# Performance work log

Hardware: AMD Instinct MI355X
Metric: run time of the kernel (lower is better)

## Reference

```python
import jax, jax.numpy as jnp
import numpy as np

# --- quantization helpers (I-BERT-style symmetric quantization) ---

def _quant_int(x, scale, bit):
    # round(x/scale) clamped to signed `bit`-bit range (SymmetricQuantFunction)
    n = 2 ** (bit - 1) - 1
    return jnp.clip(jnp.round(x / scale), -n - 1, n)


def quant_linear(x, s_x, W, b, weight_bit=8):
    """QuantLinear: per-output-channel symmetric 8-bit weight quant, int GEMM, dequant.
    Returns (output, bias_scaling_factor[out_features])."""
    n = 2 ** (weight_bit - 1) - 1
    w_scale = jnp.maximum(jnp.max(jnp.abs(W), axis=1), 1e-8) / n          # (out,)
    w_int = _quant_int(W, w_scale[:, None], weight_bit)                   # int-valued (out,in)
    b_scale = w_scale * s_x                                               # (out,) broadcasts with scalar s_x
    b_int = jnp.round(b / b_scale)                                        # 32-bit bias, no clamp needed
    x_int = x / s_x                                                       # int-valued activations
    out_int = jnp.einsum('bsi,oi->bso', x_int, w_int) + b_int
    return out_int * b_scale, b_scale


def quant_act(x, bit):
    """QuantAct: per-tensor symmetric requantization to `bit` bits (dynamic min/max)."""
    n = 2 ** (bit - 1) - 1
    scale = jnp.maximum(jnp.max(jnp.abs(x)), 1e-8) / n                    # scalar
    x_int = _quant_int(x, scale, bit)
    return x_int * scale, scale


def int_gelu(x, s):
    """IntGELU (I-BERT): integer 2nd-order polynomial approximation of erf."""
    k = 1.4142
    c0, c1 = -0.2888, -1.769
    c2 = 1.0 / c0
    SHIFT = 14  # 'const' in the original code

    x_int = x / s
    se = s / k  # scaling factor fed to int_erf
    # --- int_erf ---
    b_int = jnp.floor(c1 / se)
    c_int = jnp.floor(c2 / se ** 2)
    sign = jnp.sign(x_int)
    abs_int = jnp.minimum(jnp.abs(x_int), -b_int)
    y_int = sign * ((abs_int + b_int) ** 2 + c_int)
    se2 = se ** 2 * c0
    y_int = jnp.floor(y_int / 2 ** SHIFT)
    se2 = se2 * 2 ** SHIFT
    # --- gelu = x * (erf/2 + 1/2) in integer form ---
    shift_int = jnp.floor(1.0 / se2)
    out_int = x_int * (y_int + shift_int)
    s_out = s * se2 / 2
    return out_int * s_out, s_out


def setup_inputs() -> dict:
    key = jax.random.key(0)
    k_x, k_w1, k_b1, k_w2, k_b2 = jax.random.split(key, 5)
    B, S, D, H = 8, 1024, 768, 3072
    x = jax.random.normal(k_x, (B, S, D), dtype=jnp.float32)
    act_scaling_factor = jnp.full((1,), 0.02, dtype=jnp.float32)
    # pre-quantize x onto its input grid (x arrives already quantized in the real pipeline)
    x = jnp.round(x / act_scaling_factor) * act_scaling_factor
    W1 = jax.random.normal(k_w1, (H, D), dtype=jnp.float32) * 0.02
    b1 = jax.random.normal(k_b1, (H,), dtype=jnp.float32) * 0.02
    W2 = jax.random.normal(k_w2, (D, H), dtype=jnp.float32) * 0.02
    b2 = jax.random.normal(k_b2, (D,), dtype=jnp.float32) * 0.02
    return {"x": x, "act_scaling_factor": act_scaling_factor,
            "W1": W1, "b1": b1, "W2": W2, "b2": b2}


def reference(x, act_scaling_factor, W1, b1, W2, b2):
    s = act_scaling_factor
    h, s = quant_linear(x, s, W1, b1)       # fc1: int8 GEMM + dequant
    h, s = quant_act(h, 8)                  # qact_gelu
    h, s = int_gelu(h, s)                   # IntGELU
    h, s = quant_act(h, 8)                  # qact1 (drop=0.0 -> identity)
    h, s = quant_linear(h, s, W2, b2)       # fc2
    h, s = quant_act(h, 16)                 # qact2 (16-bit)
    return h, s
```

## Files before the change

kernel.cpp:

```cpp
#include <hip/hip_runtime.h>

typedef _Float16 half8  __attribute__((ext_vector_type(8)));
typedef _Float16 half4v __attribute__((ext_vector_type(4)));
typedef unsigned short ushort8 __attribute__((ext_vector_type(8)));
typedef float f32x4 __attribute__((ext_vector_type(4)));

#define M_DIM 8192
#define D_DIM 768
#define H_DIM 3072

#define WS_WSCALE2   16
#define WS_BINT1     (WS_WSCALE2 + 768*4)
#define WS_BSCALE1   (WS_BINT1 + 3072*4)
#define WS_BINT2     (WS_BSCALE1 + 3072*4)
#define WS_BSCALE2   (WS_BINT2 + 768*4)
#define WS_LUT       (WS_BSCALE2 + 768*4)
#define WS_XQ        34560UL
#define WS_WQ1       (WS_XQ  + (size_t)M_DIM*D_DIM*2)
#define WS_WQ2       (WS_WQ1 + (size_t)H_DIM*D_DIM*2)
#define WS_H1        (WS_WQ2 + (size_t)D_DIM*H_DIM*2)
#define WS_XQ2       WS_H1
#define WS_Q1        (WS_H1 + (size_t)M_DIM*H_DIM*4)
#define WS_H2        WS_Q1

__device__ __forceinline__ void gl_lds16(const _Float16* g, _Float16* l) {
  __builtin_amdgcn_global_load_lds(
      (const __attribute__((address_space(1))) void*)g,
      (__attribute__((address_space(3))) void*)l, 16, 0, 0);
}

struct GeluP { float scale1, bintg, cintg, shiftint, s_out; };

__device__ __forceinline__ GeluP gelu_params(float max1) {
  GeluP p;
  p.scale1 = fmaxf(max1, 1e-8f) / 127.0f;
  float se = p.scale1 / 1.4142f;
  p.bintg = floorf(-1.769f / se);
  p.cintg = floorf(((float)(1.0 / -0.2888)) / (se * se));
  float se2 = ((se * se) * -0.2888f) * 16384.0f;
  p.shiftint = floorf(1.0f / se2);
  p.s_out = (p.scale1 * se2) * 0.5f;
  return p;
}

__device__ __forceinline__ float gelu_val(const GeluP& p, float qf) {
  float sg = (qf > 0.f) ? 1.f : ((qf < 0.f) ? -1.f : 0.f);
  float aq = fminf(fabsf(qf), -p.bintg);
  float t = aq + p.bintg;
  float y = sg * (t * t + p.cintg);
  float yf = floorf(y * (1.0f / 16384.0f));
  return (qf * (yf + p.shiftint)) * p.s_out;
}

__global__ __launch_bounds__(256)
void k1_prep(const float* __restrict__ W1, const float* __restrict__ b1,
             const float* __restrict__ W2, const float* __restrict__ sxp,
             _Float16* __restrict__ wq1, _Float16* __restrict__ wq2,
             float* __restrict__ wscale2, float* __restrict__ bint1,
             float* __restrict__ bscale1, unsigned* __restrict__ wsu)
{
  if (blockIdx.x == 0 && threadIdx.x == 0) { wsu[0] = 0u; wsu[1] = 0u; wsu[2] = 0u; }
  int w = blockIdx.x * 4 + (threadIdx.x >> 6);
  int lane = threadIdx.x & 63;
  if (w < H_DIM) {
    const float* row = W1 + (size_t)w * D_DIM;
    f32x4 v[3]; float m = 0.f;
#pragma unroll
    for (int t = 0; t < 3; t++) {
      v[t] = *(const f32x4*)(row + t * 256 + lane * 4);
#pragma unroll
      for (int j = 0; j < 4; j++) m = fmaxf(m, fabsf(v[t][j]));
    }
#pragma unroll
    for (int off = 32; off >= 1; off >>= 1) m = fmaxf(m, __shfl_xor(m, off));
    float wsc = fmaxf(m, 1e-8f) / 127.0f;
    _Float16* orow = wq1 + (size_t)w * D_DIM;
#pragma unroll
    for (int t = 0; t < 3; t++) {
      half4v h;
#pragma unroll
      for (int j = 0; j < 4; j++) {
        float q = fminf(fmaxf(rintf(v[t][j] / wsc), -128.f), 127.f);
        h[j] = (_Float16)q;
      }
      *(half4v*)(orow + t * 256 + lane * 4) = h;
    }
    if (lane == 0) {
      float bs = wsc * sxp[0];
      bint1[w] = rintf(b1[w] / bs);
      bscale1[w] = bs;
    }
  } else {
    int o = w - H_DIM;
    const float* row = W2 + (size_t)o * H_DIM;
    f32x4 v[12]; float m = 0.f;
#pragma unroll
    for (int t = 0; t < 12; t++) {
      v[t] = *(const f32x4*)(row + t * 256 + lane * 4);
#pragma unroll
      for (int j = 0; j < 4; j++) m = fmaxf(m, fabsf(v[t][j]));
    }
#pragma unroll
    for (int off = 32; off >= 1; off >>= 1) m = fmaxf(m, __shfl_xor(m, off));
    float wsc = fmaxf(m, 1e-8f) / 127.0f;
    _Float16* orow = wq2 + (size_t)o * H_DIM;
#pragma unroll
    for (int t = 0; t < 12; t++) {
      half4v h;
#pragma unroll
      for (int j = 0; j < 4; j++) {
        float q = fminf(fmaxf(rintf(v[t][j] / wsc), -128.f), 127.f);
        h[j] = (_Float16)q;
      }
      *(half4v*)(orow + t * 256 + lane * 4) = h;
    }
    if (lane == 0) wscale2[o] = wsc;
  }
}

__global__ __launch_bounds__(256)
void k2_quant_x(const float* __restrict__ x, const float* __restrict__ sxp,
                _Float16* __restrict__ xq, int n4)
{
  float sx = sxp[0];
  int stride = gridDim.x * blockDim.x;
  for (int i = blockIdx.x * blockDim.x + threadIdx.x; i < n4; i += stride) {
    f32x4 v = ((const f32x4*)x)[i];
    half4v h;
#pragma unroll
    for (int j = 0; j < 4; j++) h[j] = (_Float16)(v[j] / sx);
    ((half4v*)xq)[i] = h;
  }
}

__global__ __launch_bounds__(256)
void gemm_q(const _Float16* __restrict__ A, const _Float16* __restrict__ B,
            const float* __restrict__ bint, const float* __restrict__ bscale,
            float* __restrict__ C, unsigned* __restrict__ maxw, int N, int K)
{
  __shared__ _Float16 sA[128 * 32];
  __shared__ _Float16 sB[128 * 32];
  __shared__ float wred[4];
  const int tid = threadIdx.x;
  const int wid = tid >> 6;
  const int lane = tid & 63;
  const int m0 = blockIdx.x * 128;
  const int n0 = blockIdx.y * 128;
  const int wr = (wid >> 1) * 64;
  const int wc = (wid & 1) * 64;
  const int lrow = lane & 15;
  const int lk = (lane >> 4) * 8;
  const int srow = lane >> 2;
  const int schunk = (lane & 3) * 8;

  const _Float16* Ab = A + (size_t)m0 * K;
  const _Float16* Bb = B + (size_t)n0 * K;

  f32x4 acc[4][4];
#pragma unroll
  for (int i = 0; i < 4; i++)
#pragma unroll
    for (int j = 0; j < 4; j++) acc[i][j] = (f32x4){0.f, 0.f, 0.f, 0.f};

  for (int k0 = 0; k0 < K; k0 += 32) {
#pragma unroll
    for (int r = 0; r < 2; r++) {
      const int rq = r * 4 + wid;
      const int row = rq * 16 + srow;
      gl_lds16(Ab + (size_t)row * K + (k0 + schunk), sA + rq * 512);
      gl_lds16(Bb + (size_t)row * K + (k0 + schunk), sB + rq * 512);
    }
    __syncthreads();
    half8 a[4], b[4];
#pragma unroll
    for (int f = 0; f < 4; f++) {
      a[f] = *(const half8*)&sA[(wr + f * 16 + lrow) * 32 + lk];
      b[f] = *(const half8*)&sB[(wc + f * 16 + lrow) * 32 + lk];
    }
#pragma unroll
    for (int i = 0; i < 4; i++)
#pragma unroll
      for (int j = 0; j < 4; j++)
        acc[i][j] = __builtin_amdgcn_mfma_f32_16x16x32_f16(a[i], b[j], acc[i][j], 0, 0, 0);
    __syncthreads();
  }

  float tmax = 0.f;
  const int orow0 = m0 + wr + (lane >> 4) * 4;
  const int ocol0 = n0 + wc + lrow;
#pragma unroll
  for (int j = 0; j < 4; j++) {
    const int col = ocol0 + j * 16;
    const float bi = bint[col];
    const float bs = bscale[col];
#pragma unroll
    for (int i = 0; i < 4; i++) {
#pragma unroll
      for (int e = 0; e < 4; e++) {
        const int rowm = orow0 + i * 16 + e;
        float v = (acc[i][j][e] + bi) * bs;
        C[(size_t)rowm * N + col] = v;
        tmax = fmaxf(tmax, fabsf(v));
      }
    }
  }
#pragma unroll
  for (int off = 32; off >= 1; off >>= 1) tmax = fmaxf(tmax, __shfl_xor(tmax, off));
  if (lane == 0) wred[wid] = tmax;
  __syncthreads();
  if (tid == 0) {
    float bm = fmaxf(fmaxf(wred[0], wred[1]), fmaxf(wred[2], wred[3]));
    atomicMax(maxw, __float_as_uint(bm));
  }
}

__global__ __launch_bounds__(256)
void k4_gelu(const float* __restrict__ h1, const unsigned* __restrict__ wsu,
             char* __restrict__ q1, unsigned* __restrict__ maxw, int n4)
{
  GeluP p = gelu_params(__uint_as_float(wsu[0]));
  float tmax = 0.f;
  int stride = gridDim.x * blockDim.x;
  for (int i = blockIdx.x * blockDim.x + threadIdx.x; i < n4; i += stride) {
    f32x4 h = ((const f32x4*)h1)[i];
    unsigned pack = 0;
#pragma unroll
    for (int j = 0; j < 4; j++) {
      float qf = fminf(fmaxf(rintf(h[j] / p.scale1), -128.f), 127.f);
      tmax = fmaxf(tmax, fabsf(gelu_val(p, qf)));
      pack |= ((unsigned)(unsigned char)(char)(int)qf) << (8 * j);
    }
    ((unsigned*)q1)[i] = pack;
  }
#pragma unroll
  for (int off = 32; off >= 1; off >>= 1) tmax = fmaxf(tmax, __shfl_xor(tmax, off));
  __shared__ float wred[4];
  int wid = threadIdx.x >> 6;
  if ((threadIdx.x & 63) == 0) wred[wid] = tmax;
  __syncthreads();
  if (threadIdx.x == 0) {
    float bm = fmaxf(fmaxf(wred[0], wred[1]), fmaxf(wred[2], wred[3]));
    atomicMax(maxw, __float_as_uint(bm));
  }
}

__global__ __launch_bounds__(256)
void k45_lut(const unsigned* __restrict__ wsu, const float* __restrict__ wscale2,
             const float* __restrict__ b2, unsigned short* __restrict__ lut,
             float* __restrict__ bint2, float* __restrict__ bscale2)
{
  GeluP p = gelu_params(__uint_as_float(wsu[0]));
  float scale2 = fmaxf(__uint_as_float(wsu[1]), 1e-8f) / 127.0f;
  int tid = threadIdx.x;
  {
    float qf = (float)(tid - 128);
    float g = gelu_val(p, qf);
    float q2 = fminf(fmaxf(rintf(g / scale2), -128.f), 127.f);
    _Float16 hv = (_Float16)q2;
    unsigned short u; __builtin_memcpy(&u, &hv, 2);
    lut[tid] = u;
  }
  for (int o = tid; o < D_DIM; o += 256) {
    float bs = wscale2[o] * scale2;
    bint2[o] = rintf(b2[o] / bs);
    bscale2[o] = bs;
  }
}

__global__ __launch_bounds__(256)
void k5_x2(const char* __restrict__ q1, const unsigned short* __restrict__ lutg,
           _Float16* __restrict__ xq2, int n8)
{
  __shared__ unsigned short lut[256];
  lut[threadIdx.x] = lutg[threadIdx.x];
  __syncthreads();
  int stride = gridDim.x * blockDim.x;
  for (int i = blockIdx.x * blockDim.x + threadIdx.x; i < n8; i += stride) {
    uint2 pk = ((const uint2*)q1)[i];
    ushort8 o;
#pragma unroll
    for (int j = 0; j < 4; j++) o[j]     = lut[(int)(signed char)(pk.x >> (8 * j)) + 128];
#pragma unroll
    for (int j = 0; j < 4; j++) o[4 + j] = lut[(int)(signed char)(pk.y >> (8 * j)) + 128];
    ((ushort8*)xq2)[i] = o;
  }
}

__global__ __launch_bounds__(256)
void k7_final(const float* __restrict__ h2, const unsigned* __restrict__ wsu,
              float* __restrict__ out, int n4, int ntot)
{
  float scale16 = fmaxf(__uint_as_float(wsu[2]), 1e-8f) / 32767.0f;
  int stride = gridDim.x * blockDim.x;
  for (int i = blockIdx.x * blockDim.x + threadIdx.x; i < n4; i += stride) {
    f32x4 v = ((const f32x4*)h2)[i];
    f32x4 o;
#pragma unroll
    for (int j = 0; j < 4; j++) {
      float q = fminf(fmaxf(rintf(v[j] / scale16), -32768.f), 32767.f);
      o[j] = q * scale16;
    }
    ((f32x4*)out)[i] = o;
  }
  if (blockIdx.x == 0 && threadIdx.x == 0) out[ntot] = scale16;
}

extern "C" void kernel_launch(void* const* d_in, const int* in_sizes, int n_in,
                              void* d_out, int out_size, void* d_ws, size_t ws_size,
                              hipStream_t stream)
{
  (void)in_sizes; (void)n_in; (void)out_size; (void)ws_size;
  const float* x  = (const float*)d_in[0];
  const float* sx = (const float*)d_in[1];
  const float* W1 = (const float*)d_in[2];
  const float* b1 = (const float*)d_in[3];
  const float* W2 = (const float*)d_in[4];
  const float* b2 = (const float*)d_in[5];
  float* out = (float*)d_out;
  char* ws = (char*)d_ws;

  unsigned* wsu      = (unsigned*)ws;
  float* wscale2     = (float*)(ws + WS_WSCALE2);
  float* bint1       = (float*)(ws + WS_BINT1);
  float* bscale1     = (float*)(ws + WS_BSCALE1);
  float* bint2       = (float*)(ws + WS_BINT2);
  float* bscale2     = (float*)(ws + WS_BSCALE2);
  unsigned short* lut= (unsigned short*)(ws + WS_LUT);
  _Float16* xq  = (_Float16*)(ws + WS_XQ);
  _Float16* wq1 = (_Float16*)(ws + WS_WQ1);
  _Float16* wq2 = (_Float16*)(ws + WS_WQ2);
  float* h1     = (float*)(ws + WS_H1);
  _Float16* xq2 = (_Float16*)(ws + WS_XQ2);
  char* q1      = (char*)(ws + WS_Q1);
  float* h2     = (float*)(ws + WS_H2);

  k1_prep<<<dim3(960), dim3(256), 0, stream>>>(W1, b1, W2, sx, wq1, wq2, wscale2, bint1, bscale1, wsu);
  k2_quant_x<<<dim3(2048), dim3(256), 0, stream>>>(x, sx, xq, (M_DIM * D_DIM) / 4);
  gemm_q<<<dim3(64, 24), dim3(256), 0, stream>>>(xq, wq1, bint1, bscale1, h1, wsu + 0, H_DIM, D_DIM);
  k4_gelu<<<dim3(2048), dim3(256), 0, stream>>>(h1, wsu, q1, wsu + 1, (M_DIM * H_DIM) / 4);
  k45_lut<<<dim3(1), dim3(256), 0, stream>>>(wsu, wscale2, b2, lut, bint2, bscale2);
  k5_x2<<<dim3(2048), dim3(256), 0, stream>>>(q1, lut, xq2, (M_DIM * H_DIM) / 8);
  gemm_q<<<dim3(64, 6), dim3(256), 0, stream>>>(xq2, wq2, bint2, bscale2, h2, wsu + 2, D_DIM, H_DIM);
  k7_final<<<dim3(2048), dim3(256), 0, stream>>>(h2, wsu, out, (M_DIM * D_DIM) / 4, M_DIM * D_DIM);
}
```

Measured before the change: 221.6 us.

## Switch second GEMM to int8 MFMA and double-buffer both GEMMs' LDS staging

Stores W2 and the requantized GELU activations as int8 rather than fp16, and runs fc2 with the i32_16x16x64_i8 MFMA using a 64x128 tile. The GELU lookup table is replaced by direct per-element GELU requantization into int8 bytes. Both GEMMs now double-buffer their global-to-LDS loads so the next K-slice is fetched while the current one is multiplied. This halves the bytes moved for the fc2 operands and uses the denser int8 MFMA rate, at the cost of more ALU work in the requant kernel and a smaller tile for fc2.

```diff
diff --git a/kernel.cpp b/kernel.cpp
--- a/kernel.cpp
+++ b/kernel.cpp
@@ -2,8 +2,8 @@
 
 typedef _Float16 half8  __attribute__((ext_vector_type(8)));
 typedef _Float16 half4v __attribute__((ext_vector_type(4)));
-typedef unsigned short ushort8 __attribute__((ext_vector_type(8)));
 typedef float f32x4 __attribute__((ext_vector_type(4)));
+typedef int int4v __attribute__((ext_vector_type(4)));
 
 #define M_DIM 8192
 #define D_DIM 768
@@ -14,16 +14,20 @@
 #define WS_BSCALE1   (WS_BINT1 + 3072*4)
 #define WS_BINT2     (WS_BSCALE1 + 3072*4)
 #define WS_BSCALE2   (WS_BINT2 + 768*4)
-#define WS_LUT       (WS_BSCALE2 + 768*4)
 #define WS_XQ        34560UL
 #define WS_WQ1       (WS_XQ  + (size_t)M_DIM*D_DIM*2)
-#define WS_WQ2       (WS_WQ1 + (size_t)H_DIM*D_DIM*2)
-#define WS_H1        (WS_WQ2 + (size_t)D_DIM*H_DIM*2)
-#define WS_XQ2       WS_H1
+#define WS_WQ2I      (WS_WQ1 + (size_t)H_DIM*D_DIM*2)
+#define WS_H1        (WS_WQ2I + (size_t)D_DIM*H_DIM)
+#define WS_Q2        WS_H1
+#define WS_H2        (WS_H1 + (size_t)M_DIM*H_DIM)
 #define WS_Q1        (WS_H1 + (size_t)M_DIM*H_DIM*4)
-#define WS_H2        WS_Q1
 
 __device__ __forceinline__ void gl_lds16(const _Float16* g, _Float16* l) {
+  __builtin_amdgcn_global_load_lds(
+      (const __attribute__((address_space(1))) void*)g,
+      (__attribute__((address_space(3))) void*)l, 16, 0, 0);
+}
+__device__ __forceinline__ void gl_lds16c(const char* g, char* l) {
   __builtin_amdgcn_global_load_lds(
       (const __attribute__((address_space(1))) void*)g,
       (__attribute__((address_space(3))) void*)l, 16, 0, 0);
@@ -55,7 +59,7 @@
 __global__ __launch_bounds__(256)
 void k1_prep(const float* __restrict__ W1, const float* __restrict__ b1,
              const float* __restrict__ W2, const float* __restrict__ sxp,
-             _Float16* __restrict__ wq1, _Float16* __restrict__ wq2,
+             _Float16* __restrict__ wq1, char* __restrict__ wq2i,
              float* __restrict__ wscale2, float* __restrict__ bint1,
              float* __restrict__ bscale1, unsigned* __restrict__ wsu)
 {
@@ -103,16 +107,16 @@
 #pragma unroll
     for (int off = 32; off >= 1; off >>= 1) m = fmaxf(m, __shfl_xor(m, off));
     float wsc = fmaxf(m, 1e-8f) / 127.0f;
-    _Float16* orow = wq2 + (size_t)o * H_DIM;
+    unsigned* orow = (unsigned*)(wq2i + (size_t)o * H_DIM);
 #pragma unroll
     for (int t = 0; t < 12; t++) {
-      half4v h;
+      unsigned pk = 0;
 #pragma unroll
       for (int j = 0; j < 4; j++) {
         float q = fminf(fmaxf(rintf(v[t][j] / wsc), -128.f), 127.f);
-        h[j] = (_Float16)q;
+        pk |= ((unsigned)(unsigned char)(char)(int)q) << (8 * j);
       }
-      *(half4v*)(orow + t * 256 + lane * 4) = h;
+      orow[t * 64 + lane] = pk;
     }
     if (lane == 0) wscale2[o] = wsc;
   }
@@ -134,12 +138,12 @@
 }
 
 __global__ __launch_bounds__(256)
-void gemm_q(const _Float16* __restrict__ A, const _Float16* __restrict__ B,
-            const float* __restrict__ bint, const float* __restrict__ bscale,
-            float* __restrict__ C, unsigned* __restrict__ maxw, int N, int K)
-{
-  __shared__ _Float16 sA[128 * 32];
-  __shared__ _Float16 sB[128 * 32];
+void gemm_f16(const _Float16* __restrict__ A, const _Float16* __restrict__ B,
+              const float* __restrict__ bint, const float* __restrict__ bscale,
+              float* __restrict__ C, unsigned* __restrict__ maxw, int N, int K)
+{
+  __shared__ _Float16 sA[2][128 * 32];
+  __shared__ _Float16 sB[2][128 * 32];
   __shared__ float wred[4];
   const int tid = threadIdx.x;
   const int wid = tid >> 6;
@@ -162,20 +166,28 @@
 #pragma unroll
     for (int j = 0; j < 4; j++) acc[i][j] = (f32x4){0.f, 0.f, 0.f, 0.f};
 
-  for (int k0 = 0; k0 < K; k0 += 32) {
-#pragma unroll
-    for (int r = 0; r < 2; r++) {
-      const int rq = r * 4 + wid;
-      const int row = rq * 16 + srow;
-      gl_lds16(Ab + (size_t)row * K + (k0 + schunk), sA + rq * 512);
-      gl_lds16(Bb + (size_t)row * K + (k0 + schunk), sB + rq * 512);
-    }
-    __syncthreads();
+  const int nt = K / 32;
+
+#define STAGE_F16(bufi, k0) do {                                              \
+    _Float16* dA = sA[bufi]; _Float16* dB = sB[bufi];                         \
+    _Pragma("unroll")                                                         \
+    for (int r = 0; r < 2; r++) {                                             \
+      const int rq = r * 4 + wid;                                             \
+      const int row = rq * 16 + srow;                                         \
+      gl_lds16(Ab + (size_t)row * K + ((k0) + schunk), dA + rq * 512);        \
+      gl_lds16(Bb + (size_t)row * K + ((k0) + schunk), dB + rq * 512);        \
+    } } while (0)
+
+  STAGE_F16(0, 0);
+  __syncthreads();
+  int cur = 0;
+  for (int t = 0; t < nt; ++t) {
+    if (t + 1 < nt) STAGE_F16(cur ^ 1, (t + 1) * 32);
     half8 a[4], b[4];
 #pragma unroll
     for (int f = 0; f < 4; f++) {
-      a[f] = *(const half8*)&sA[(wr + f * 16 + lrow) * 32 + lk];
-      b[f] = *(const half8*)&sB[(wc + f * 16 + lrow) * 32 + lk];
+      a[f] = *(const half8*)&sA[cur][(wr + f * 16 + lrow) * 32 + lk];
+      b[f] = *(const half8*)&sB[cur][(wc + f * 16 + lrow) * 32 + lk];
     }
 #pragma unroll
     for (int i = 0; i < 4; i++)
@@ -183,7 +195,9 @@
       for (int j = 0; j < 4; j++)
         acc[i][j] = __builtin_amdgcn_mfma_f32_16x16x32_f16(a[i], b[j], acc[i][j], 0, 0, 0);
     __syncthreads();
-  }
+    cur ^= 1;
+  }
+#undef STAGE_F16
 
   float tmax = 0.f;
   const int orow0 = m0 + wr + (lane >> 4) * 4;
@@ -245,22 +259,12 @@
 }
 
 __global__ __launch_bounds__(256)
-void k45_lut(const unsigned* __restrict__ wsu, const float* __restrict__ wscale2,
-             const float* __restrict__ b2, unsigned short* __restrict__ lut,
-             float* __restrict__ bint2, float* __restrict__ bscale2)
-{
-  GeluP p = gelu_params(__uint_as_float(wsu[0]));
+void k6_bias(const unsigned* __restrict__ wsu, const float* __restrict__ wscale2,
+             const float* __restrict__ b2, float* __restrict__ bint2,
+             float* __restrict__ bscale2)
+{
   float scale2 = fmaxf(__uint_as_float(wsu[1]), 1e-8f) / 127.0f;
-  int tid = threadIdx.x;
-  {
-    float qf = (float)(tid - 128);
-    float g = gelu_val(p, qf);
-    float q2 = fminf(fmaxf(rintf(g / scale2), -128.f), 127.f);
-    _Float16 hv = (_Float16)q2;
-    unsigned short u; __builtin_memcpy(&u, &hv, 2);
-    lut[tid] = u;
-  }
-  for (int o = tid; o < D_DIM; o += 256) {
+  for (int o = threadIdx.x; o < D_DIM; o += 256) {
     float bs = wscale2[o] * scale2;
     bint2[o] = rintf(b2[o] / bs);
     bscale2[o] = bs;
@@ -268,21 +272,123 @@
 }
 
 __global__ __launch_bounds__(256)
-void k5_x2(const char* __restrict__ q1, const unsigned short* __restrict__ lutg,
-           _Float16* __restrict__ xq2, int n8)
-{
-  __shared__ unsigned short lut[256];
-  lut[threadIdx.x] = lutg[threadIdx.x];
+void k5_q2(const char* __restrict__ q1, const unsigned* __restrict__ wsu,
+           char* __restrict__ q2, int n16)
+{
+  GeluP p = gelu_params(__uint_as_float(wsu[0]));
+  float scale2 = fmaxf(__uint_as_float(wsu[1]), 1e-8f) / 127.0f;
+  int stride = gridDim.x * blockDim.x;
+  for (int i = blockIdx.x * blockDim.x + threadIdx.x; i < n16; i += stride) {
+    uint4 pk = ((const uint4*)q1)[i];
+    uint4 o;
+    unsigned* pw[4] = {&o.x, &o.y, &o.z, &o.w};
+    unsigned pr[4] = {pk.x, pk.y, pk.z, pk.w};
+#pragma unroll
+    for (int w = 0; w < 4; w++) {
+      unsigned acc = 0;
+#pragma unroll
+      for (int j = 0; j < 4; j++) {
+        float qf = (float)(int)(signed char)(pr[w] >> (8 * j));
+        float g = gelu_val(p, qf);
+        float q2f = fminf(fmaxf(rintf(g / scale2), -128.f), 127.f);
+        acc |= ((unsigned)(unsigned char)(char)(int)q2f) << (8 * j);
+      }
+      *pw[w] = acc;
+    }
+    ((uint4*)q2)[i] = o;
+  }
+}
+
+__global__ __launch_bounds__(256)
+void gemm_i8(const char* __restrict__ A, const char* __restrict__ B,
+             const float* __restrict__ bint, const float* __restrict__ bscale,
+             float* __restrict__ C, unsigned* __restrict__ maxw, int N, int K)
+{
+  __shared__ char sA[2][64 * 64];
+  __shared__ char sB[2][128 * 64];
+  __shared__ float wred[4];
+  const int tid = threadIdx.x;
+  const int wid = tid >> 6;
+  const int lane = tid & 63;
+  const int m0 = blockIdx.x * 64;
+  const int n0 = blockIdx.y * 128;
+  const int wr = (wid >> 1) * 32;
+  const int wc = (wid & 1) * 64;
+  const int lrow = lane & 15;
+  const int lkc = (lane >> 4) * 16;
+  const int srow = lane >> 2;
+  const int schunk = (lane & 3) * 16;
+
+  const char* Ab = A + (size_t)m0 * K;
+  const char* Bb = B + (size_t)n0 * K;
+
+  int4v acc[2][4];
+#pragma unroll
+  for (int i = 0; i < 2; i++)
+#pragma unroll
+    for (int j = 0; j < 4; j++) acc[i][j] = (int4v){0, 0, 0, 0};
+
+  const int nt = K / 64;
+
+#define STAGE_I8(bufi, k0) do {                                               \
+    char* dA = sA[bufi]; char* dB = sB[bufi];                                 \
+    gl_lds16c(Ab + (size_t)(wid * 16 + srow) * K + ((k0) + schunk),           \
+              dA + wid * 1024);                                               \
+    _Pragma("unroll")                                                         \
+    for (int r = 0; r < 2; r++) {                                             \
+      const int rq = r * 4 + wid;                                             \
+      gl_lds16c(Bb + (size_t)(rq * 16 + srow) * K + ((k0) + schunk),          \
+                dB + rq * 1024);                                              \
+    } } while (0)
+
+  STAGE_I8(0, 0);
   __syncthreads();
-  int stride = gridDim.x * blockDim.x;
-  for (int i = blockIdx.x * blockDim.x + threadIdx.x; i < n8; i += stride) {
-    uint2 pk = ((const uint2*)q1)[i];
-    ushort8 o;
-#pragma unroll
-    for (int j = 0; j < 4; j++) o[j]     = lut[(int)(signed char)(pk.x >> (8 * j)) + 128];
-#pragma unroll
-    for (int j = 0; j < 4; j++) o[4 + j] = lut[(int)(signed char)(pk.y >> (8 * j)) + 128];
-    ((ushort8*)xq2)[i] = o;
+  int cur = 0;
+  for (int t = 0; t < nt; ++t) {
+    if (t + 1 < nt) STAGE_I8(cur ^ 1, (t + 1) * 64);
+    int4v a[2], b[4];
+#pragma unroll
+    for (int f = 0; f < 2; f++)
+      a[f] = *(const int4v*)&sA[cur][(wr + f * 16 + lrow) * 64 + lkc];
+#pragma unroll
+    for (int f = 0; f < 4; f++)
+      b[f] = *(const int4v*)&sB[cur][(wc + f * 16 + lrow) * 64 + lkc];
+#pragma unroll
+    for (int i = 0; i < 2; i++)
+#pragma unroll
+      for (int j = 0; j < 4; j++)
+        acc[i][j] = __builtin_amdgcn_mfma_i32_16x16x64_i8(a[i], b[j], acc[i][j], 0, 0, 0);
+    __syncthreads();
+    cur ^= 1;
+  }
+#undef STAGE_I8
+
+  float tmax = 0.f;
+  const int orow0 = m0 + wr + (lane >> 4) * 4;
+  const int ocol0 = n0 + wc + lrow;
+#pragma unroll
+  for (int j = 0; j < 4; j++) {
+    const int col = ocol0 + j * 16;
+    const float bi = bint[col];
+    const float bs = bscale[col];
+#pragma unroll
+    for (int i = 0; i < 2; i++) {
+#pragma unroll
+      for (int e = 0; e < 4; e++) {
+        const int rowm = orow0 + i * 16 + e;
+        float v = ((float)acc[i][j][e] + bi) * bs;
+        C[(size_t)rowm * N + col] = v;
+        tmax = fmaxf(tmax, fabsf(v));
+      }
+    }
+  }
+#pragma unroll
+  for (int off = 32; off >= 1; off >>= 1) tmax = fmaxf(tmax, __shfl_xor(tmax, off));
+  if (lane == 0) wred[wid] = tmax;
+  __syncthreads();
+  if (tid == 0) {
+    float bm = fmaxf(fmaxf(wred[0], wred[1]), fmaxf(wred[2], wred[3]));
+    atomicMax(maxw, __float_as_uint(bm));
   }
 }
 
@@ -319,27 +425,26 @@
   float* out = (float*)d_out;
   char* ws = (char*)d_ws;
 
-  unsigned* wsu      = (unsigned*)ws;
-  float* wscale2     = (float*)(ws + WS_WSCALE2);
-  float* bint1       = (float*)(ws + WS_BINT1);
-  float* bscale1     = (float*)(ws + WS_BSCALE1);
-  float* bint2       = (float*)(ws + WS_BINT2);
-  float* bscale2     = (float*)(ws + WS_BSCALE2);
-  unsigned short* lut= (unsigned short*)(ws + WS_LUT);
-  _Float16* xq  = (_Float16*)(ws + WS_XQ);
-  _Float16* wq1 = (_Float16*)(ws + WS_WQ1);
-  _Float16* wq2 = (_Float16*)(ws + WS_WQ2);
-  float* h1     = (float*)(ws + WS_H1);
-  _Float16* xq2 = (_Float16*)(ws + WS_XQ2);
-  char* q1      = (char*)(ws + WS_Q1);
-  float* h2     = (float*)(ws + WS_H2);
-
-  k1_prep<<<dim3(960), dim3(256), 0, stream>>>(W1, b1, W2, sx, wq1, wq2, wscale2, bint1, bscale1, wsu);
+  unsigned* wsu   = (unsigned*)ws;
+  float* wscale2  = (float*)(ws + WS_WSCALE2);
+  float* bint1    = (float*)(ws + WS_BINT1);
+  float* bscale1  = (float*)(ws + WS_BSCALE1);
+  float* bint2    = (float*)(ws + WS_BINT2);
+  float* bscale2  = (float*)(ws + WS_BSCALE2);
+  _Float16* xq    = (_Float16*)(ws + WS_XQ);
+  _Float16* wq1   = (_Float16*)(ws + WS_WQ1);
+  char* wq2i      = (char*)(ws + WS_WQ2I);
+  float* h1       = (float*)(ws + WS_H1);
+  char* q2        = (char*)(ws + WS_Q2);
+  float* h2       = (float*)(ws + WS_H2);
+  char* q1        = (char*)(ws + WS_Q1);
+
+  k1_prep<<<dim3(960), dim3(256), 0, stream>>>(W1, b1, W2, sx, wq1, wq2i, wscale2, bint1, bscale1, wsu);
   k2_quant_x<<<dim3(2048), dim3(256), 0, stream>>>(x, sx, xq, (M_DIM * D_DIM) / 4);
-  gemm_q<<<dim3(64, 24), dim3(256), 0, stream>>>(xq, wq1, bint1, bscale1, h1, wsu + 0, H_DIM, D_DIM);
+  gemm_f16<<<dim3(64, 24), dim3(256), 0, stream>>>(xq, wq1, bint1, bscale1, h1, wsu + 0, H_DIM, D_DIM);
   k4_gelu<<<dim3(2048), dim3(256), 0, stream>>>(h1, wsu, q1, wsu + 1, (M_DIM * H_DIM) / 4);
-  k45_lut<<<dim3(1), dim3(256), 0, stream>>>(wsu, wscale2, b2, lut, bint2, bscale2);
-  k5_x2<<<dim3(2048), dim3(256), 0, stream>>>(q1, lut, xq2, (M_DIM * H_DIM) / 8);
-  gemm_q<<<dim3(64, 6), dim3(256), 0, stream>>>(xq2, wq2, bint2, bscale2, h2, wsu + 2, D_DIM, H_DIM);
+  k6_bias<<<dim3(1), dim3(256), 0, stream>>>(wsu, wscale2, b2, bint2, bscale2);
+  k5_q2<<<dim3(2048), dim3(256), 0, stream>>>(q1, wsu, q2, (M_DIM * H_DIM) / 16);
+  gemm_i8<<<dim3(128, 6), dim3(256), 0, stream>>>(q2, wq2i, bint2, bscale2, h2, wsu + 2, D_DIM, H_DIM);
   k7_final<<<dim3(2048), dim3(256), 0, stream>>>(h2, wsu, out, (M_DIM * D_DIM) / 4, M_DIM * D_DIM);
 }
```

After: 195.9 us. -11.6%, faster.
